# Kernel optimization log

Measured on AMD Instinct MI355X. Metric: run time of the kernel, lower is better.

Reference implementation:

```python
import jax, jax.numpy as jnp
import numpy as np

HEADS, DH, RS = 8, 32, 16  # heads, dim_head, reduce_size

def _dwconv(x, w):
    # depthwise 3x3, pad=1, stride=1 (OIHW with I=1, groups=C)
    return jax.lax.conv_general_dilated(x, w, (1, 1), [(1, 1), (1, 1)],
        dimension_numbers=('NCHW', 'OIHW', 'NCHW'), feature_group_count=x.shape[1])

def _pwconv(x, w):
    return jax.lax.conv_general_dilated(x, w, (1, 1), 'VALID',
        dimension_numbers=('NCHW', 'OIHW', 'NCHW'))

def _bilinear_ac(x, oh, ow):
    # F.interpolate(mode='bilinear', align_corners=True)
    B, C, H, W = x.shape
    ys = jnp.linspace(0., H - 1., oh)
    xs = jnp.linspace(0., W - 1., ow)
    y0 = jnp.floor(ys).astype(jnp.int32); y1 = jnp.minimum(y0 + 1, H - 1)
    x0 = jnp.floor(xs).astype(jnp.int32); x1 = jnp.minimum(x0 + 1, W - 1)
    wy = (ys - y0)[None, None, :, None]
    wx = (xs - x0)[None, None, None, :]
    top = x[:, :, y0, :] * (1. - wy) + x[:, :, y1, :] * wy
    return top[:, :, :, x0] * (1. - wx) + top[:, :, :, x1] * wx

def _ln(t, g, b, eps=1e-6):
    # per-head LayerNorm over last dim; g,b: [heads, dim_head]
    mu = t.mean(-1, keepdims=True)
    var = ((t - mu) ** 2).mean(-1, keepdims=True)
    return (t - mu) / jnp.sqrt(var + eps) * g[None, :, None, :] + b[None, :, None, :]

def setup_inputs() -> dict:
    key = jax.random.key(0)
    ks = jax.random.split(key, 6)
    C = HEADS * DH  # 256
    x = jax.random.normal(ks[0], (8, C, 64, 64), jnp.float32)
    qkv_dw = jax.random.normal(ks[1], (C, 1, 3, 3), jnp.float32) * 0.05
    qkv_pw = jax.random.normal(ks[2], (3 * C, C, 1, 1), jnp.float32) * 0.05
    out_dw = jax.random.normal(ks[3], (C, 1, 3, 3), jnp.float32) * 0.05
    out_pw = jax.random.normal(ks[4], (C, C, 1, 1), jnp.float32) * 0.05
    gq = jnp.ones((HEADS, DH), jnp.float32); bq = jnp.zeros((HEADS, DH), jnp.float32)
    gk = jnp.ones((HEADS, DH), jnp.float32); bk = jnp.zeros((HEADS, DH), jnp.float32)
    bias_table = jax.random.normal(ks[5], ((2 * RS - 1) * (2 * RS - 1), HEADS), jnp.float32) * 0.02
    # relative_position_index buffer, exactly as in RelativePositionBias.__init__
    coords = np.stack(np.meshgrid(np.arange(RS), np.arange(RS), indexing='ij')).reshape(2, -1)
    rel = (coords[:, :, None] - coords[:, None, :]).transpose(1, 2, 0).copy()
    rel[:, :, 0] += RS - 1; rel[:, :, 1] += RS - 1; rel[:, :, 0] *= 2 * RS - 1
    rel_index = jnp.asarray(rel.sum(-1), jnp.int32)  # [RS*RS, RS*RS]
    return dict(x=x, qkv_dw=qkv_dw, qkv_pw=qkv_pw, out_dw=out_dw, out_pw=out_pw,
                gq=gq, bq=bq, gk=gk, bk=bk, bias_table=bias_table, rel_index=rel_index)

def reference(x, qkv_dw, qkv_pw, out_dw, out_pw, gq, bq, gk, bk, bias_table, rel_index):
    B, C, H, W = x.shape
    qkv = _pwconv(_dwconv(x, qkv_dw), qkv_pw)          # [B, 3*inner_dim, H, W]
    q, k, v = jnp.split(qkv, 3, axis=1)
    k = _bilinear_ac(k, RS, RS)
    v = _bilinear_ac(v, RS, RS)
    def heads(t):  # 'b (dim_head heads) h w -> b heads (h w) dim_head'
        b, _, hh, ww = t.shape
        return t.reshape(b, DH, HEADS, hh * ww).transpose(0, 2, 3, 1)
    q = _ln(heads(q), gq, bq)                           # [B, h, H*W, DH]
    k = _ln(heads(k), gk, bk)                           # [B, h, RS*RS, DH]
    v = heads(v)
    attn = jnp.einsum('bhid,bhjd->bhij', q, k)          # [B, h, H*W, RS*RS]
    # relative position bias: gather + repeat_interleave expansion
    bias = bias_table[rel_index.reshape(-1)].reshape(RS, RS, RS * RS, HEADS)
    bias = jnp.repeat(jnp.repeat(bias, H // RS, axis=0), W // RS, axis=1)
    bias = bias.reshape(H * W, RS * RS, HEADS).transpose(2, 0, 1)[None]
    attn = (attn + bias) * (1.0 / DH)                   # scale = dim_head ** -1 (no softmax)
    out = jnp.einsum('bhij,bhjd->bhid', attn, v)        # [B, h, H*W, DH]
    out = out.reshape(B, HEADS, H, W, DH).transpose(0, 4, 1, 2, 3).reshape(B, DH * HEADS, H, W)
    out = _pwconv(_dwconv(out, out_dw), out_pw)
    return out, attn
```

## Files before the change

### kernel.cpp

```cpp
#include <hip/hip_runtime.h>
#include <cstdint>

#define HW_ 4096

typedef __attribute__((ext_vector_type(8))) short bf16x8;
typedef __attribute__((ext_vector_type(4))) short bf16x4;
typedef __attribute__((ext_vector_type(4))) float f32x4;

static __device__ __forceinline__ unsigned short f2bf(float f) {
  unsigned u = __builtin_bit_cast(unsigned, f);
  u += 0x7FFF + ((u >> 16) & 1);
  return (unsigned short)(u >> 16);
}
static __device__ __forceinline__ float bf2f(unsigned short u) {
  return __builtin_bit_cast(float, (unsigned)u << 16);
}
static __device__ __forceinline__ float ldf(const float* p) { return *p; }
static __device__ __forceinline__ float ldf(const unsigned short* p) { return bf2f(*p); }

static __device__ __forceinline__ void gl_lds16(const unsigned short* g,
                                                unsigned short* s) {
  __builtin_amdgcn_global_load_lds(
      (const __attribute__((address_space(1))) unsigned int*)g,
      (__attribute__((address_space(3))) unsigned int*)s, 16, 0, 0);
}

template <typename T, int DO_PREP>
__global__ __launch_bounds__(256) void dwconv_t_kernel(
    const T* __restrict__ x, const float* __restrict__ w9,
    unsigned short* __restrict__ xT,
    const float* __restrict__ pw1, const float* __restrict__ pw2,
    unsigned short* __restrict__ wb, const float* __restrict__ btab,
    const int* __restrict__ relidx, float* __restrict__ bias_pre) {
  if (DO_PREP && blockIdx.z == 8) {
    int idx0 = (blockIdx.y * 64 + blockIdx.x) * 256 + threadIdx.x;
#pragma unroll
    for (int k = 0; k < 12; ++k) {
      int idx = idx0 + k * 65536;
      if (idx < 65536) {
        wb[idx] = f2bf(pw1[idx]);
      } else if (idx < 131072) {
        int t = idx - 65536;
        int row = t >> 8, col = t & 255;
        int h = row >> 5, d = row & 31;
        wb[idx] = f2bf(pw1[(256 + d * 8 + h) * 256 + col]);
      } else if (idx < 196608) {
        int t = idx - 131072;
        int row = t >> 8, col = t & 255;
        int h = row >> 5, d = row & 31;
        wb[idx] = f2bf(pw1[(512 + d * 8 + h) * 256 + col]);
      } else if (idx < 262144) {
        wb[idx] = f2bf(pw2[idx - 196608]);
      } else {
        int t = idx - 262144;
        int j = t & 255, g = (t >> 8) & 255, h = t >> 16;
        bias_pre[t] = btab[relidx[g * 256 + j] * 8 + h] * 0.03125f;
      }
    }
    return;
  }
  __shared__ unsigned short lds_t[64][66];
  int iy = blockIdx.x;
  int cg = blockIdx.y;
  int b  = blockIdx.z;
  int tid = threadIdx.x;
  int px  = tid & 63;
  int cl0 = (tid >> 6) * 16;
  const T* xrow = x + (size_t)b * 256 * HW_ + iy * 64 + px;
#pragma unroll 4
  for (int e = 0; e < 16; ++e) {
    int c = cg * 64 + cl0 + e;
    const T* xp = xrow + (size_t)c * HW_;
    const float* wp = w9 + c * 9;
    float v0 = (iy > 0)  ? ldf(xp - 64) : 0.f;
    float v1 = ldf(xp);
    float v2 = (iy < 63) ? ldf(xp + 64) : 0.f;
    float l0 = __shfl(v0, px - 1, 64), r0 = __shfl(v0, px + 1, 64);
    float l1 = __shfl(v1, px - 1, 64), r1 = __shfl(v1, px + 1, 64);
    float l2 = __shfl(v2, px - 1, 64), r2 = __shfl(v2, px + 1, 64);
    if (px == 0)  { l0 = 0.f; l1 = 0.f; l2 = 0.f; }
    if (px == 63) { r0 = 0.f; r1 = 0.f; r2 = 0.f; }
    float acc = l0 * wp[0] + v0 * wp[1] + r0 * wp[2]
              + l1 * wp[3] + v1 * wp[4] + r1 * wp[5]
              + l2 * wp[6] + v2 * wp[7] + r2 * wp[8];
    lds_t[cl0 + e][px] = f2bf(acc);
  }
  __syncthreads();
#pragma unroll
  for (int j = 0; j < 2; ++j) {
    int flat = tid + j * 256;
    int rpx = flat >> 3, cseg = flat & 7;
    unsigned v0 = (unsigned)lds_t[cseg*8+0][rpx] | ((unsigned)lds_t[cseg*8+1][rpx] << 16);
    unsigned v1 = (unsigned)lds_t[cseg*8+2][rpx] | ((unsigned)lds_t[cseg*8+3][rpx] << 16);
    unsigned v2 = (unsigned)lds_t[cseg*8+4][rpx] | ((unsigned)lds_t[cseg*8+5][rpx] << 16);
    unsigned v3 = (unsigned)lds_t[cseg*8+6][rpx] | ((unsigned)lds_t[cseg*8+7][rpx] << 16);
    uint4 pk = {v0, v1, v2, v3};
    *(uint4*)(xT + ((size_t)b * 4096 + iy * 64 + rpx) * 256 + cg * 64 + cseg * 8) = pk;
  }
}

template <int OUT_BF16, int KV>
__global__ __launch_bounds__(256) void pwconv_mfma_kernel(
    const unsigned short* __restrict__ XT, const unsigned short* __restrict__ W,
    void* __restrict__ Yv, int OC, unsigned short* __restrict__ xds) {
  __shared__ unsigned short smem[18432];
  unsigned short* As = smem;
  unsigned short* Bs = smem + 8192;
  int tid = threadIdx.x;
  int b = blockIdx.z;
  if (KV && blockIdx.y == 2) {
    if (blockIdx.x >= 8) return;
    int j0 = blockIdx.x * 32;
    int jloc = tid >> 3, icg = tid & 7;
    int j = j0 + jloc;
    int oy = j >> 4, ox = j & 15;
    const float s = 63.0f / 15.0f;
    float ys = oy * s, xf = ox * s;
    int y0 = (int)ys, x0 = (int)xf;
    int y1 = min(y0 + 1, 63), x1 = min(x0 + 1, 63);
    float wy = ys - (float)y0, wx = xf - (float)x0;
    float w00 = (1.f - wy) * (1.f - wx), w01 = (1.f - wy) * wx;
    float w10 = wy * (1.f - wx), w11 = wy * wx;
    const unsigned short* base = XT + (size_t)b * 4096 * 256 + icg * 32;
    const bf16x8* p00 = (const bf16x8*)(base + (size_t)(y0 * 64 + x0) * 256);
    const bf16x8* p01 = (const bf16x8*)(base + (size_t)(y0 * 64 + x1) * 256);
    const bf16x8* p10 = (const bf16x8*)(base + (size_t)(y1 * 64 + x0) * 256);
    const bf16x8* p11 = (const bf16x8*)(base + (size_t)(y1 * 64 + x1) * 256);
    unsigned short* xo = xds + ((size_t)(b * 256 + j)) * 256 + icg * 32;
#pragma unroll
    for (int q = 0; q < 4; ++q) {
      bf16x8 a00 = p00[q], a01 = p01[q], a10 = p10[q], a11 = p11[q];
      unsigned rp[4];
#pragma unroll
      for (int e2 = 0; e2 < 4; ++e2) {
        float f0 = w00 * bf2f((unsigned short)a00[2*e2])   + w01 * bf2f((unsigned short)a01[2*e2])
                 + w10 * bf2f((unsigned short)a10[2*e2])   + w11 * bf2f((unsigned short)a11[2*e2]);
        float f1 = w00 * bf2f((unsigned short)a00[2*e2+1]) + w01 * bf2f((unsigned short)a01[2*e2+1])
                 + w10 * bf2f((unsigned short)a10[2*e2+1]) + w11 * bf2f((unsigned short)a11[2*e2+1]);
        rp[e2] = (unsigned)f2bf(f0) | ((unsigned)f2bf(f1) << 16);
      }
      uint4 pk = {rp[0], rp[1], rp[2], rp[3]};
      *(uint4*)(xo + q * 8) = pk;
    }
    return;
  }
  int oc0 = blockIdx.y * 128, p0 = blockIdx.x * 128;
  int w = tid >> 6, l = tid & 63;
  int wm = w >> 1, wn = w & 1;
  int lr = l & 15, lg = l >> 4;
  const unsigned short* Wp = W + (size_t)oc0 * 256;
  const unsigned short* Xp = XT + ((size_t)b * 4096 + p0) * 256;
  f32x4 acc[4][4] = {};
  for (int kt = 0; kt < 4; ++kt) {
    int k0 = kt * 64;
#pragma unroll
    for (int j = 0; j < 4; ++j) {
      int chunk = w * 4 + j;
      int row = chunk * 8 + (l >> 3);
      int lcu = (l & 7) ^ (row & 7);
      gl_lds16(Wp + (size_t)row * 256 + k0 + lcu * 8, &As[chunk * 512]);
      gl_lds16(Xp + (size_t)row * 256 + k0 + lcu * 8, &Bs[chunk * 512]);
    }
    __syncthreads();
#pragma unroll
    for (int ks = 0; ks < 2; ++ks) {
      bf16x8 af[4], bfr[4];
      int ku = ks * 4 + lg;
#pragma unroll
      for (int mi = 0; mi < 4; ++mi) {
        int row = wm * 64 + mi * 16 + lr;
        af[mi] = *(const bf16x8*)&As[row * 64 + (ku ^ (row & 7)) * 8];
      }
#pragma unroll
      for (int ni = 0; ni < 4; ++ni) {
        int row = wn * 64 + ni * 16 + lr;
        bfr[ni] = *(const bf16x8*)&Bs[row * 64 + (ku ^ (row & 7)) * 8];
      }
#pragma unroll
      for (int mi = 0; mi < 4; ++mi)
#pragma unroll
        for (int ni = 0; ni < 4; ++ni)
          acc[mi][ni] = __builtin_amdgcn_mfma_f32_16x16x32_bf16(
              af[mi], bfr[ni], acc[mi][ni], 0, 0, 0);
    }
    __syncthreads();
  }
  if constexpr (OUT_BF16) {
    unsigned short (*Cs)[136] = (unsigned short(*)[136])smem;
#pragma unroll
    for (int mi = 0; mi < 4; ++mi)
#pragma unroll
      for (int ni = 0; ni < 4; ++ni)
#pragma unroll
        for (int r = 0; r < 4; ++r)
          Cs[wm * 64 + mi * 16 + lg * 4 + r][wn * 64 + ni * 16 + lr] =
              f2bf(acc[mi][ni][r]);
    __syncthreads();
    unsigned short* Yb = (unsigned short*)Yv + (size_t)b * OC * HW_;
    int pc = tid & 15, ocr = tid >> 4;
#pragma unroll
    for (int it = 0; it < 8; ++it) {
      int oc = it * 16 + ocr;
      uint4 pk = *(const uint4*)&Cs[oc][pc * 8];
      *(uint4*)(Yb + (size_t)(oc0 + oc) * HW_ + p0 + pc * 8) = pk;
    }
  } else {
    float* Yb = (float*)Yv + (size_t)b * OC * HW_;
#pragma unroll
    for (int mi = 0; mi < 4; ++mi)
#pragma unroll
      for (int ni = 0; ni < 4; ++ni)
#pragma unroll
        for (int r = 0; r < 4; ++r) {
          int oc = oc0 + wm * 64 + mi * 16 + lg * 4 + r;
          int p  = p0 + wn * 64 + ni * 16 + lr;
          Yb[(size_t)oc * HW_ + p] = acc[mi][ni][r];
        }
  }
}

__global__ __launch_bounds__(256) void kv_gemm_kernel(
    const unsigned short* __restrict__ XDS, const unsigned short* __restrict__ W,
    const float* __restrict__ gk, const float* __restrict__ bk,
    unsigned short* __restrict__ kln, unsigned short* __restrict__ vfrag) {
  __shared__ unsigned short smem[18432];
  unsigned short* As = smem;
  unsigned short* Bs = smem + 8192;
  int tid = threadIdx.x;
  int b = blockIdx.z, yv = blockIdx.y;
  int oc0 = yv * 128, p0 = blockIdx.x * 128;
  int w = tid >> 6, l = tid & 63;
  int wm = w >> 1, wn = w & 1;
  int lr = l & 15, lg = l >> 4;
  const unsigned short* Wp = W + (size_t)oc0 * 256;
  const unsigned short* Xp = XDS + ((size_t)b * 256 + p0) * 256;
  f32x4 acc[4][4] = {};
  for (int kt = 0; kt < 4; ++kt) {
    int k0 = kt * 64;
#pragma unroll
    for (int j = 0; j < 4; ++j) {
      int chunk = w * 4 + j;
      int row = chunk * 8 + (l >> 3);
      int lcu = (l & 7) ^ (row & 7);
      gl_lds16(Wp + (size_t)row * 256 + k0 + lcu * 8, &As[chunk * 512]);
      gl_lds16(Xp + (size_t)row * 256 + k0 + lcu * 8, &Bs[chunk * 512]);
    }
    __syncthreads();
#pragma unroll
    for (int ks = 0; ks < 2; ++ks) {
      bf16x8 af[4], bfr[4];
      int ku = ks * 4 + lg;
#pragma unroll
      for (int mi = 0; mi < 4; ++mi) {
        int row = wm * 64 + mi * 16 + lr;
        af[mi] = *(const bf16x8*)&As[row * 64 + (ku ^ (row & 7)) * 8];
      }
#pragma unroll
      for (int ni = 0; ni < 4; ++ni) {
        int row = wn * 64 + ni * 16 + lr;
        bfr[ni] = *(const bf16x8*)&Bs[row * 64 + (ku ^ (row & 7)) * 8];
      }
#pragma unroll
      for (int mi = 0; mi < 4; ++mi)
#pragma unroll
        for (int ni = 0; ni < 4; ++ni)
          acc[mi][ni] = __builtin_amdgcn_mfma_f32_16x16x32_bf16(
              af[mi], bfr[ni], acc[mi][ni], 0, 0, 0);
    }
    __syncthreads();
  }
  unsigned short (*Cs)[136] = (unsigned short(*)[136])smem;
#pragma unroll
  for (int mi = 0; mi < 4; ++mi)
#pragma unroll
    for (int ni = 0; ni < 4; ++ni)
#pragma unroll
      for (int r = 0; r < 4; ++r)
        Cs[wm * 64 + mi * 16 + lg * 4 + r][wn * 64 + ni * 16 + lr] =
            f2bf(acc[mi][ni][r]);
  __syncthreads();
  int hl = tid >> 6;
  int jl = tid & 63;
  if (yv < 2) {
    int h = yv * 4 + hl;
    int bh = b * 8 + h;
#pragma unroll
    for (int jj = 0; jj < 2; ++jj) {
      int jc = jl * 2 + jj;
      int j = p0 + jc;
      float v[32];
      float s1 = 0.f, s2 = 0.f;
#pragma unroll
      for (int d = 0; d < 32; ++d) {
        v[d] = bf2f(Cs[hl * 32 + d][jc]);
        s1 += v[d]; s2 += v[d] * v[d];
      }
      float mu = s1 * (1.f / 32.f);
      float var = s2 * (1.f / 32.f) - mu * mu;
      float inv = 1.0f / sqrtf(var + 1e-6f);
      unsigned rp[16];
#pragma unroll
      for (int t = 0; t < 16; ++t) {
        float y0f = (v[2*t]   - mu) * inv * gk[h*32 + 2*t]   + bk[h*32 + 2*t];
        float y1f = (v[2*t+1] - mu) * inv * gk[h*32 + 2*t+1] + bk[h*32 + 2*t+1];
        rp[t] = (unsigned)f2bf(y0f) | ((unsigned)f2bf(y1f) << 16);
      }
      uint4* ko = (uint4*)(kln + ((size_t)bh * 256 + j) * 32);
#pragma unroll
      for (int t4 = 0; t4 < 4; ++t4) {
        uint4 pk = {rp[t4*4], rp[t4*4+1], rp[t4*4+2], rp[t4*4+3]};
        ko[t4] = pk;
      }
    }
  } else {
    int h = (yv - 2) * 4 + hl;
    int bh = b * 8 + h;
#pragma unroll
    for (int jj = 0; jj < 2; ++jj) {
      int jc = jl * 2 + jj;
      int j = p0 + jc;
      int c = j >> 4, gq2 = (j >> 2) & 3, ii = j & 3;
      unsigned short* vo = vfrag + (size_t)bh * 8192;
#pragma unroll
      for (int d = 0; d < 32; ++d) {
        int dt = d >> 4, dr = d & 15;
        vo[(c * 2 + dt) * 256 + (gq2 * 16 + dr) * 4 + ii] = Cs[hl * 32 + d][jc];
      }
    }
  }
}

__global__ __launch_bounds__(256) void attn_mfma_kernel(
    const unsigned short* __restrict__ qb, const float* __restrict__ gq,
    const float* __restrict__ bq, const unsigned short* __restrict__ kln,
    const unsigned short* __restrict__ vfrag, const float* __restrict__ bias_pre,
    float* __restrict__ attn_out, unsigned short* __restrict__ out_nchw) {
  __shared__ unsigned short sT[32][72];
  int tile = blockIdx.x, h = blockIdx.y, b = blockIdx.z;
  int bh = b * 8 + h;
  int tid = threadIdx.x;
  int w = tid >> 6, l = tid & 63;
  int lr = l & 15, lg = l >> 4;
  int qbase = tile * 64 + w * 16;
  int q = qbase + lr;
  int iy = q >> 6, ix = q & 63;
  int g = (iy >> 2) * 16 + (ix >> 2);

  const unsigned short* qp = qb + ((size_t)b * 256 + h) * HW_ + q;
  float qv[8];
  float sum = 0.f, sum2 = 0.f;
#pragma unroll
  for (int e = 0; e < 8; ++e) {
    qv[e] = bf2f(qp[(size_t)((lg * 8 + e) * 8) * HW_]);
    sum += qv[e]; sum2 += qv[e] * qv[e];
  }
  sum  += __shfl_xor(sum, 16, 64);  sum  += __shfl_xor(sum, 32, 64);
  sum2 += __shfl_xor(sum2, 16, 64); sum2 += __shfl_xor(sum2, 32, 64);
  float mu = sum * (1.f / 32.f);
  float var = sum2 * (1.f / 32.f) - mu * mu;
  float inv = 1.0f / sqrtf(var + 1e-6f);
  bf16x8 qf;
#pragma unroll
  for (int e = 0; e < 8; ++e) {
    int d = lg * 8 + e;
    float y = (qv[e] - mu) * inv * gq[h * 32 + d] + bq[h * 32 + d];
    qf[e] = (short)f2bf(y);
  }

  const unsigned short* kbase = kln + (size_t)bh * 256 * 32 + lr * 32 + lg * 8;
  const unsigned short* vbase = vfrag + (size_t)bh * 32 * 256 + l * 4;
  const float* bbase = bias_pre + ((size_t)h * 256 + g) * 256 + lg * 4;
  float* abase = attn_out + ((size_t)bh * 4096 + q) * 256 + lg * 4;

  f32x4 z = {0.f, 0.f, 0.f, 0.f};
  f32x4 oacc0 = z, oacc1 = z;
#pragma unroll
  for (int c = 0; c < 16; ++c) {
    bf16x8 kf = *(const bf16x8*)(kbase + c * 16 * 32);
    f32x4 s = __builtin_amdgcn_mfma_f32_16x16x32_bf16(kf, qf, z, 0, 0, 0);
    f32x4 bias = *(const f32x4*)(bbase + c * 16);
    f32x4 t = s * 0.03125f + bias;
    __builtin_nontemporal_store(t, (f32x4*)(abase + c * 16));
    bf16x4 pb;
    pb[0] = (short)f2bf(t.x);
    pb[1] = (short)f2bf(t.y);
    pb[2] = (short)f2bf(t.z);
    pb[3] = (short)f2bf(t.w);
    bf16x4 va0 = *(const bf16x4*)(vbase + (c * 2 + 0) * 256);
    bf16x4 va1 = *(const bf16x4*)(vbase + (c * 2 + 1) * 256);
    oacc0 = __builtin_amdgcn_mfma_f32_16x16x16bf16_1k(va0, pb, oacc0, 0, 0, 0);
    oacc1 = __builtin_amdgcn_mfma_f32_16x16x16bf16_1k(va1, pb, oacc1, 0, 0, 0);
  }
  float ov[8] = {oacc0.x, oacc0.y, oacc0.z, oacc0.w,
                 oacc1.x, oacc1.y, oacc1.z, oacc1.w};
#pragma unroll
  for (int dt = 0; dt < 2; ++dt)
#pragma unroll
    for (int r = 0; r < 4; ++r)
      sT[dt * 16 + lg * 4 + r][w * 16 + lr] = f2bf(ov[dt * 4 + r]);
  __syncthreads();
  {
    int row = tid >> 3, seg = tid & 7;
    uint4 pk = *(const uint4*)&sT[row][seg * 8];
    int cc = row * 8 + h;
    *(uint4*)(out_nchw + ((size_t)b * 256 + cc) * HW_ + tile * 64 + seg * 8) = pk;
  }
}

extern "C" void kernel_launch(void* const* d_in, const int* in_sizes, int n_in,
                              void* d_out, int out_size, void* d_ws, size_t ws_size,
                              hipStream_t stream) {
  const float* x      = (const float*)d_in[0];
  const float* qkv_dw = (const float*)d_in[1];
  const float* qkv_pw = (const float*)d_in[2];
  const float* out_dw = (const float*)d_in[3];
  const float* out_pw = (const float*)d_in[4];
  const float* gq     = (const float*)d_in[5];
  const float* bq     = (const float*)d_in[6];
  const float* gk     = (const float*)d_in[7];
  const float* bk     = (const float*)d_in[8];
  const float* btab   = (const float*)d_in[9];
  const int*   relidx = (const int*)d_in[10];

  float* out  = (float*)d_out;
  float* attn = out + 8388608;

  unsigned short* us = (unsigned short*)d_ws;
  unsigned short* xT1    = us;
  unsigned short* xT2    = us + 8388608;
  unsigned short* onchwb = us + 16777216;
  unsigned short* kln    = us + 25165824;
  unsigned short* vfrag  = us + 25690112;
  unsigned short* wbuf   = us + 26214400;
  float* bias_pre = (float*)(us + 26476544);
  unsigned short* qb     = us + 27525120;
  unsigned short* xds    = us + 35913728;

  dwconv_t_kernel<float, 1><<<dim3(64, 4, 9), 256, 0, stream>>>(
      x, qkv_dw, xT1, qkv_pw, out_pw, wbuf, btab, relidx, bias_pre);
  pwconv_mfma_kernel<1, 1><<<dim3(32, 3, 8), 256, 0, stream>>>(
      xT1, wbuf, qb, 256, xds);
  kv_gemm_kernel<<<dim3(2, 4, 8), 256, 0, stream>>>(
      xds, wbuf + 65536, gk, bk, kln, vfrag);
  attn_mfma_kernel<<<dim3(64, 8, 8), 256, 0, stream>>>(qb, gq, bq, kln, vfrag,
                                                       bias_pre, attn, onchwb);
  dwconv_t_kernel<unsigned short, 0><<<dim3(64, 4, 8), 256, 0, stream>>>(
      onchwb, out_dw, xT2, nullptr, nullptr, nullptr, nullptr, nullptr, nullptr);
  pwconv_mfma_kernel<0, 0><<<dim3(32, 2, 8), 256, 0, stream>>>(
      xT2, wbuf + 196608, out, 256, nullptr);
}
```

Before: 149.1 us.

## Fuse bilinear downsample and K/V GEMM into the QKV pwconv kernel

The K/V path no longer writes a downsampled bf16 buffer and runs a separate GEMM kernel. Blocks with blockIdx.y==2 now compute the bilinear samples on the fly into the LDS B tile, then run the K/V MFMA GEMM plus LayerNorm and the V fragment scatter in the same launch. This removes one kernel launch and the intermediate global round trip. The cost is that K/V work (8 blocks per batch) runs alongside the q GEMM, with scalar-computed B-tile staging in place of async global-to-LDS loads.

```diff
diff --git a/kernel.cpp b/kernel.cpp
--- a/kernel.cpp
+++ b/kernel.cpp
@@ -102,7 +102,9 @@
 template <int OUT_BF16, int KV>
 __global__ __launch_bounds__(256) void pwconv_mfma_kernel(
     const unsigned short* __restrict__ XT, const unsigned short* __restrict__ W,
-    void* __restrict__ Yv, int OC, unsigned short* __restrict__ xds) {
+    void* __restrict__ Yv, int OC,
+    const float* __restrict__ gk, const float* __restrict__ bk,
+    unsigned short* __restrict__ kln, unsigned short* __restrict__ vfrag) {
   __shared__ unsigned short smem[18432];
   unsigned short* As = smem;
   unsigned short* Bs = smem + 8192;
@@ -110,37 +112,135 @@
   int b = blockIdx.z;
   if (KV && blockIdx.y == 2) {
     if (blockIdx.x >= 8) return;
-    int j0 = blockIdx.x * 32;
-    int jloc = tid >> 3, icg = tid & 7;
-    int j = j0 + jloc;
-    int oy = j >> 4, ox = j & 15;
-    const float s = 63.0f / 15.0f;
-    float ys = oy * s, xf = ox * s;
-    int y0 = (int)ys, x0 = (int)xf;
-    int y1 = min(y0 + 1, 63), x1 = min(x0 + 1, 63);
-    float wy = ys - (float)y0, wx = xf - (float)x0;
-    float w00 = (1.f - wy) * (1.f - wx), w01 = (1.f - wy) * wx;
-    float w10 = wy * (1.f - wx), w11 = wy * wx;
-    const unsigned short* base = XT + (size_t)b * 4096 * 256 + icg * 32;
-    const bf16x8* p00 = (const bf16x8*)(base + (size_t)(y0 * 64 + x0) * 256);
-    const bf16x8* p01 = (const bf16x8*)(base + (size_t)(y0 * 64 + x1) * 256);
-    const bf16x8* p10 = (const bf16x8*)(base + (size_t)(y1 * 64 + x0) * 256);
-    const bf16x8* p11 = (const bf16x8*)(base + (size_t)(y1 * 64 + x1) * 256);
-    unsigned short* xo = xds + ((size_t)(b * 256 + j)) * 256 + icg * 32;
-#pragma unroll
-    for (int q = 0; q < 4; ++q) {
-      bf16x8 a00 = p00[q], a01 = p01[q], a10 = p10[q], a11 = p11[q];
-      unsigned rp[4];
-#pragma unroll
-      for (int e2 = 0; e2 < 4; ++e2) {
-        float f0 = w00 * bf2f((unsigned short)a00[2*e2])   + w01 * bf2f((unsigned short)a01[2*e2])
-                 + w10 * bf2f((unsigned short)a10[2*e2])   + w11 * bf2f((unsigned short)a11[2*e2]);
-        float f1 = w00 * bf2f((unsigned short)a00[2*e2+1]) + w01 * bf2f((unsigned short)a01[2*e2+1])
-                 + w10 * bf2f((unsigned short)a10[2*e2+1]) + w11 * bf2f((unsigned short)a11[2*e2+1]);
-        rp[e2] = (unsigned)f2bf(f0) | ((unsigned)f2bf(f1) << 16);
-      }
-      uint4 pk = {rp[0], rp[1], rp[2], rp[3]};
-      *(uint4*)(xo + q * 8) = pk;
+    int oc_t = blockIdx.x >> 1, p_t = blockIdx.x & 1;
+    int oc0 = oc_t * 128, p0 = p_t * 128;
+    const unsigned short* Wp = W + 65536 + (size_t)oc0 * 256;
+    const unsigned short* xb = XT + (size_t)b * 4096 * 256;
+    int w = tid >> 6, l = tid & 63;
+    int wm = w >> 1, wn = w & 1;
+    int lr = l & 15, lg = l >> 4;
+    f32x4 acc[4][4] = {};
+    for (int kt = 0; kt < 4; ++kt) {
+      int k0 = kt * 64;
+#pragma unroll
+      for (int j = 0; j < 4; ++j) {
+        int chunk = w * 4 + j;
+        int row = chunk * 8 + (l >> 3);
+        int lcu = (l & 7) ^ (row & 7);
+        gl_lds16(Wp + (size_t)row * 256 + k0 + lcu * 8, &As[chunk * 512]);
+      }
+#pragma unroll
+      for (int t = 0; t < 4; ++t) {
+        int unit = tid + t * 256;
+        int jloc = unit >> 3, icq = unit & 7;
+        int j = p0 + jloc;
+        int oy = j >> 4, ox = j & 15;
+        const float s = 63.0f / 15.0f;
+        float ys = oy * s, xf = ox * s;
+        int y0 = (int)ys, x0 = (int)xf;
+        int y1 = min(y0 + 1, 63), x1 = min(x0 + 1, 63);
+        float wy = ys - (float)y0, wx = xf - (float)x0;
+        float w00 = (1.f - wy) * (1.f - wx), w01 = (1.f - wy) * wx;
+        float w10 = wy * (1.f - wx), w11 = wy * wx;
+        const unsigned short* bse = xb + k0 + icq * 8;
+        bf16x8 a00 = *(const bf16x8*)(bse + (size_t)(y0 * 64 + x0) * 256);
+        bf16x8 a01 = *(const bf16x8*)(bse + (size_t)(y0 * 64 + x1) * 256);
+        bf16x8 a10 = *(const bf16x8*)(bse + (size_t)(y1 * 64 + x0) * 256);
+        bf16x8 a11 = *(const bf16x8*)(bse + (size_t)(y1 * 64 + x1) * 256);
+        unsigned rp[4];
+#pragma unroll
+        for (int e2 = 0; e2 < 4; ++e2) {
+          float f0 = w00 * bf2f((unsigned short)a00[2*e2])   + w01 * bf2f((unsigned short)a01[2*e2])
+                   + w10 * bf2f((unsigned short)a10[2*e2])   + w11 * bf2f((unsigned short)a11[2*e2]);
+          float f1 = w00 * bf2f((unsigned short)a00[2*e2+1]) + w01 * bf2f((unsigned short)a01[2*e2+1])
+                   + w10 * bf2f((unsigned short)a10[2*e2+1]) + w11 * bf2f((unsigned short)a11[2*e2+1]);
+          rp[e2] = (unsigned)f2bf(f0) | ((unsigned)f2bf(f1) << 16);
+        }
+        uint4 pk = {rp[0], rp[1], rp[2], rp[3]};
+        *(uint4*)&Bs[jloc * 64 + ((icq ^ (jloc & 7)) * 8)] = pk;
+      }
+      __syncthreads();
+#pragma unroll
+      for (int ks = 0; ks < 2; ++ks) {
+        int ku = ks * 4 + lg;
+        bf16x8 af[4], bfr[4];
+#pragma unroll
+        for (int mi = 0; mi < 4; ++mi) {
+          int row = wm * 64 + mi * 16 + lr;
+          af[mi] = *(const bf16x8*)&As[row * 64 + (ku ^ (row & 7)) * 8];
+        }
+#pragma unroll
+        for (int ni = 0; ni < 4; ++ni) {
+          int row = wn * 64 + ni * 16 + lr;
+          bfr[ni] = *(const bf16x8*)&Bs[row * 64 + (ku ^ (row & 7)) * 8];
+        }
+#pragma unroll
+        for (int mi = 0; mi < 4; ++mi)
+#pragma unroll
+          for (int ni = 0; ni < 4; ++ni)
+            acc[mi][ni] = __builtin_amdgcn_mfma_f32_16x16x32_bf16(
+                af[mi], bfr[ni], acc[mi][ni], 0, 0, 0);
+      }
+      __syncthreads();
+    }
+    unsigned short (*Cs)[136] = (unsigned short(*)[136])smem;
+#pragma unroll
+    for (int mi = 0; mi < 4; ++mi)
+#pragma unroll
+      for (int ni = 0; ni < 4; ++ni)
+#pragma unroll
+        for (int r = 0; r < 4; ++r)
+          Cs[wm * 64 + mi * 16 + lg * 4 + r][wn * 64 + ni * 16 + lr] =
+              f2bf(acc[mi][ni][r]);
+    __syncthreads();
+    int hl = tid >> 6;
+    int jl = tid & 63;
+    if (oc_t < 2) {
+      int h = oc_t * 4 + hl;
+      int bh = b * 8 + h;
+#pragma unroll
+      for (int jj = 0; jj < 2; ++jj) {
+        int jc = jl * 2 + jj;
+        int j = p0 + jc;
+        float v[32];
+        float s1 = 0.f, s2 = 0.f;
+#pragma unroll
+        for (int d = 0; d < 32; ++d) {
+          v[d] = bf2f(Cs[hl * 32 + d][jc]);
+          s1 += v[d]; s2 += v[d] * v[d];
+        }
+        float mu = s1 * (1.f / 32.f);
+        float var = s2 * (1.f / 32.f) - mu * mu;
+        float inv = 1.0f / sqrtf(var + 1e-6f);
+        unsigned rp[16];
+#pragma unroll
+        for (int t = 0; t < 16; ++t) {
+          float y0f = (v[2*t]   - mu) * inv * gk[h*32 + 2*t]   + bk[h*32 + 2*t];
+          float y1f = (v[2*t+1] - mu) * inv * gk[h*32 + 2*t+1] + bk[h*32 + 2*t+1];
+          rp[t] = (unsigned)f2bf(y0f) | ((unsigned)f2bf(y1f) << 16);
+        }
+        uint4* ko = (uint4*)(kln + ((size_t)bh * 256 + j) * 32);
+#pragma unroll
+        for (int t4 = 0; t4 < 4; ++t4) {
+          uint4 pk = {rp[t4*4], rp[t4*4+1], rp[t4*4+2], rp[t4*4+3]};
+          ko[t4] = pk;
+        }
+      }
+    } else {
+      int h = (oc_t - 2) * 4 + hl;
+      int bh = b * 8 + h;
+#pragma unroll
+      for (int jj = 0; jj < 2; ++jj) {
+        int jc = jl * 2 + jj;
+        int j = p0 + jc;
+        int c = j >> 4, gq2 = (j >> 2) & 3, ii = j & 3;
+        unsigned short* vo = vfrag + (size_t)bh * 8192;
+#pragma unroll
+        for (int d = 0; d < 32; ++d) {
+          int dt = d >> 4, dr = d & 15;
+          vo[(c * 2 + dt) * 256 + (gq2 * 16 + dr) * 4 + ii] = Cs[hl * 32 + d][jc];
+        }
+      }
     }
     return;
   }
@@ -216,117 +316,6 @@
           int p  = p0 + wn * 64 + ni * 16 + lr;
           Yb[(size_t)oc * HW_ + p] = acc[mi][ni][r];
         }
-  }
-}
-
-__global__ __launch_bounds__(256) void kv_gemm_kernel(
-    const unsigned short* __restrict__ XDS, const unsigned short* __restrict__ W,
-    const float* __restrict__ gk, const float* __restrict__ bk,
-    unsigned short* __restrict__ kln, unsigned short* __restrict__ vfrag) {
-  __shared__ unsigned short smem[18432];
-  unsigned short* As = smem;
-  unsigned short* Bs = smem + 8192;
-  int tid = threadIdx.x;
-  int b = blockIdx.z, yv = blockIdx.y;
-  int oc0 = yv * 128, p0 = blockIdx.x * 128;
-  int w = tid >> 6, l = tid & 63;
-  int wm = w >> 1, wn = w & 1;
-  int lr = l & 15, lg = l >> 4;
-  const unsigned short* Wp = W + (size_t)oc0 * 256;
-  const unsigned short* Xp = XDS + ((size_t)b * 256 + p0) * 256;
-  f32x4 acc[4][4] = {};
-  for (int kt = 0; kt < 4; ++kt) {
-    int k0 = kt * 64;
-#pragma unroll
-    for (int j = 0; j < 4; ++j) {
-      int chunk = w * 4 + j;
-      int row = chunk * 8 + (l >> 3);
-      int lcu = (l & 7) ^ (row & 7);
-      gl_lds16(Wp + (size_t)row * 256 + k0 + lcu * 8, &As[chunk * 512]);
-      gl_lds16(Xp + (size_t)row * 256 + k0 + lcu * 8, &Bs[chunk * 512]);
-    }
-    __syncthreads();
-#pragma unroll
-    for (int ks = 0; ks < 2; ++ks) {
-      bf16x8 af[4], bfr[4];
-      int ku = ks * 4 + lg;
-#pragma unroll
-      for (int mi = 0; mi < 4; ++mi) {
-        int row = wm * 64 + mi * 16 + lr;
-        af[mi] = *(const bf16x8*)&As[row * 64 + (ku ^ (row & 7)) * 8];
-      }
-#pragma unroll
-      for (int ni = 0; ni < 4; ++ni) {
-        int row = wn * 64 + ni * 16 + lr;
-        bfr[ni] = *(const bf16x8*)&Bs[row * 64 + (ku ^ (row & 7)) * 8];
-      }
-#pragma unroll
-      for (int mi = 0; mi < 4; ++mi)
-#pragma unroll
-        for (int ni = 0; ni < 4; ++ni)
-          acc[mi][ni] = __builtin_amdgcn_mfma_f32_16x16x32_bf16(
-              af[mi], bfr[ni], acc[mi][ni], 0, 0, 0);
-    }
-    __syncthreads();
-  }
-  unsigned short (*Cs)[136] = (unsigned short(*)[136])smem;
-#pragma unroll
-  for (int mi = 0; mi < 4; ++mi)
-#pragma unroll
-    for (int ni = 0; ni < 4; ++ni)
-#pragma unroll
-      for (int r = 0; r < 4; ++r)
-        Cs[wm * 64 + mi * 16 + lg * 4 + r][wn * 64 + ni * 16 + lr] =
-            f2bf(acc[mi][ni][r]);
-  __syncthreads();
-  int hl = tid >> 6;
-  int jl = tid & 63;
-  if (yv < 2) {
-    int h = yv * 4 + hl;
-    int bh = b * 8 + h;
-#pragma unroll
-    for (int jj = 0; jj < 2; ++jj) {
-      int jc = jl * 2 + jj;
-      int j = p0 + jc;
-      float v[32];
-      float s1 = 0.f, s2 = 0.f;
-#pragma unroll
-      for (int d = 0; d < 32; ++d) {
-        v[d] = bf2f(Cs[hl * 32 + d][jc]);
-        s1 += v[d]; s2 += v[d] * v[d];
-      }
-      float mu = s1 * (1.f / 32.f);
-      float var = s2 * (1.f / 32.f) - mu * mu;
-      float inv = 1.0f / sqrtf(var + 1e-6f);
-      unsigned rp[16];
-#pragma unroll
-      for (int t = 0; t < 16; ++t) {
-        float y0f = (v[2*t]   - mu) * inv * gk[h*32 + 2*t]   + bk[h*32 + 2*t];
-        float y1f = (v[2*t+1] - mu) * inv * gk[h*32 + 2*t+1] + bk[h*32 + 2*t+1];
-        rp[t] = (unsigned)f2bf(y0f) | ((unsigned)f2bf(y1f) << 16);
-      }
-      uint4* ko = (uint4*)(kln + ((size_t)bh * 256 + j) * 32);
-#pragma unroll
-      for (int t4 = 0; t4 < 4; ++t4) {
-        uint4 pk = {rp[t4*4], rp[t4*4+1], rp[t4*4+2], rp[t4*4+3]};
-        ko[t4] = pk;
-      }
-    }
-  } else {
-    int h = (yv - 2) * 4 + hl;
-    int bh = b * 8 + h;
-#pragma unroll
-    for (int jj = 0; jj < 2; ++jj) {
-      int jc = jl * 2 + jj;
-      int j = p0 + jc;
-      int c = j >> 4, gq2 = (j >> 2) & 3, ii = j & 3;
-      unsigned short* vo = vfrag + (size_t)bh * 8192;
-#pragma unroll
-      for (int d = 0; d < 32; ++d) {
-        int dt = d >> 4, dr = d & 15;
-        vo[(c * 2 + dt) * 256 + (gq2 * 16 + dr) * 4 + ii] = Cs[hl * 32 + d][jc];
-      }
-    }
   }
 }
 
@@ -434,18 +423,15 @@
   unsigned short* wbuf   = us + 26214400;
   float* bias_pre = (float*)(us + 26476544);
   unsigned short* qb     = us + 27525120;
-  unsigned short* xds    = us + 35913728;
 
   dwconv_t_kernel<float, 1><<<dim3(64, 4, 9), 256, 0, stream>>>(
       x, qkv_dw, xT1, qkv_pw, out_pw, wbuf, btab, relidx, bias_pre);
   pwconv_mfma_kernel<1, 1><<<dim3(32, 3, 8), 256, 0, stream>>>(
-      xT1, wbuf, qb, 256, xds);
-  kv_gemm_kernel<<<dim3(2, 4, 8), 256, 0, stream>>>(
-      xds, wbuf + 65536, gk, bk, kln, vfrag);
+      xT1, wbuf, qb, 256, gk, bk, kln, vfrag);
   attn_mfma_kernel<<<dim3(64, 8, 8), 256, 0, stream>>>(qb, gq, bq, kln, vfrag,
                                                        bias_pre, attn, onchwb);
   dwconv_t_kernel<unsigned short, 0><<<dim3(64, 4, 8), 256, 0, stream>>>(
       onchwb, out_dw, xT2, nullptr, nullptr, nullptr, nullptr, nullptr, nullptr);
   pwconv_mfma_kernel<0, 0><<<dim3(32, 2, 8), 256, 0, stream>>>(
-      xT2, wbuf + 196608, out, 256, nullptr);
-}
+      xT2, wbuf + 196608, out, 256, nullptr, nullptr, nullptr, nullptr);
+}
```

Result: slower. 164.1 us (+10.0%).
